# Performance work log

Measured on AMD Instinct MI355X. Metric: run time of the kernel, lower is better.

Reference implementation:

```python
import jax, jax.numpy as jnp
import numpy as np

B, S, D = 2, 2048, 2048
HQ, HK, HD = 16, 8, 128          # query heads, kv heads, head_dim
EPS = 1e-6
ROPE_THETA = 10000.0
SCALE = HD ** -0.5


def setup_inputs() -> dict:
    key = jax.random.key(0)
    ks = jax.random.split(key, 6)
    s = lambda fan_in: 1.0 / np.sqrt(fan_in)
    return {
        "hidden_states": jax.random.normal(ks[0], (B, S, D), jnp.float32),
        "positions": jnp.arange(S, dtype=jnp.int32),
        "Wq": jax.random.normal(ks[1], (D, HQ * HD), jnp.float32) * s(D),
        "Wk": jax.random.normal(ks[2], (D, HK * HD), jnp.float32) * s(D),
        "Wv": jax.random.normal(ks[3], (D, HK * HD), jnp.float32) * s(D),
        "Wo": jax.random.normal(ks[4], (HQ * HD, D), jnp.float32) * s(HQ * HD),
        "q_norm_w": jnp.ones((HD,), jnp.float32),
        "k_norm_w": jnp.ones((HD,), jnp.float32),
    }


def _rmsnorm(x, w):
    # RMSNorm over last (head_dim) axis, as in q_norm/k_norm
    var = jnp.mean(jnp.square(x), axis=-1, keepdims=True)
    return x * jax.lax.rsqrt(var + EPS) * w


def _rope(x, positions):
    # x: [B, S, H, HD]; rotate_half-style RoPE (Qwen3 convention)
    half = HD // 2
    inv_freq = 1.0 / (ROPE_THETA ** (jnp.arange(0, half, dtype=jnp.float32) / half))
    angles = positions.astype(jnp.float32)[:, None] * inv_freq[None, :]  # [S, half]
    cos = jnp.cos(angles)[None, :, None, :]  # [1, S, 1, half]
    sin = jnp.sin(angles)[None, :, None, :]
    x1, x2 = x[..., :half], x[..., half:]
    return jnp.concatenate([x1 * cos - x2 * sin, x2 * cos + x1 * sin], axis=-1)


def reference(hidden_states, positions, Wq, Wk, Wv, Wo, q_norm_w, k_norm_w):
    b, s, _ = hidden_states.shape
    q = (hidden_states @ Wq).reshape(b, s, HQ, HD)
    k = (hidden_states @ Wk).reshape(b, s, HK, HD)
    v = (hidden_states @ Wv).reshape(b, s, HK, HD)

    q = _rmsnorm(q, q_norm_w)
    k = _rmsnorm(k, k_norm_w)

    q = _rope(q, positions)
    k = _rope(k, positions)

    # GQA: repeat KV heads to match query heads
    groups = HQ // HK
    k = jnp.repeat(k, groups, axis=2)  # [B, S, HQ, HD]
    v = jnp.repeat(v, groups, axis=2)

    scores = jnp.einsum("bqhd,bkhd->bhqk", q, k) * SCALE  # [B, HQ, S, S]
    causal = jnp.tril(jnp.ones((s, s), dtype=bool))
    scores = jnp.where(causal[None, None], scores, jnp.float32(-jnp.inf))
    attn = jax.nn.softmax(scores, axis=-1)

    out = jnp.einsum("bhqk,bkhd->bqhd", attn, v).reshape(b, s, HQ * HD)
    return out @ Wo
```

## Files before the change

### kernel.cpp

```cpp
#include <hip/hip_runtime.h>
#include <cstdint>
#include <cstddef>

typedef _Float16 half8 __attribute__((ext_vector_type(8)));
typedef float f32x4 __attribute__((ext_vector_type(4)));

#define DI __device__ __forceinline__

DI void gld_lds16(void* sp, const void* gp) {
  __builtin_amdgcn_global_load_lds(
      (const __attribute__((address_space(1))) void*)gp,
      (__attribute__((address_space(3))) void*)sp, 16, 0, 0);
}

__global__ __launch_bounds__(256) void cvt_f32_f16(const float* __restrict__ in,
                                                   _Float16* __restrict__ outp, int n8) {
  const int i = blockIdx.x * 256 + threadIdx.x;
  if (i >= n8) return;
  const float4* p = (const float4*)in + (size_t)i * 2;
  const float4 a = p[0], b = p[1];
  half8 h;
  h[0] = (_Float16)a.x; h[1] = (_Float16)a.y; h[2] = (_Float16)a.z; h[3] = (_Float16)a.w;
  h[4] = (_Float16)b.x; h[5] = (_Float16)b.y; h[6] = (_Float16)b.z; h[7] = (_Float16)b.w;
  *(half8*)(outp + (size_t)i * 8) = h;
}

__global__ __launch_bounds__(256) void transpose_cvt(const float* __restrict__ in,
                                                     _Float16* __restrict__ outp,
                                                     int R, int C) {
  __shared__ float t[32][33];
  const int tx = threadIdx.x & 31, ty = threadIdx.x >> 5;
  const int ctiles = C >> 5;
  const int tc = blockIdx.x % ctiles, tr = blockIdx.x / ctiles;
  const int r0 = tr * 32, c0 = tc * 32;
#pragma unroll
  for (int i = 0; i < 4; i++)
    t[ty + 8 * i][tx] = in[(size_t)(r0 + ty + 8 * i) * C + c0 + tx];
  __syncthreads();
#pragma unroll
  for (int i = 0; i < 4; i++) {
    const int rr = ty + 8 * i;
    outp[(size_t)(c0 + rr) * R + r0 + tx] = (_Float16)t[tx][rr];
  }
}

__global__ __launch_bounds__(256) void gemm_bt(const _Float16* __restrict__ A,
                                               const _Float16* __restrict__ Bt,
                                               float* __restrict__ C,
                                               int M, int N, int K) {
  __shared__ _Float16 sA[2][128 * 32];
  __shared__ _Float16 sB[2][128 * 32];
  const int tid = threadIdx.x;
  const int w = tid >> 6, l = tid & 63, lo = l & 15, hi = l >> 4;
  const int bn0 = blockIdx.x * 128, bm0 = blockIdx.y * 128;
  const int wm = w >> 1, wn = w & 1;
  const int srow = l >> 2;
  const int scol = (l & 3) * 8;

  f32x4 acc[4][4];
#pragma unroll
  for (int mi = 0; mi < 4; mi++)
#pragma unroll
    for (int ni = 0; ni < 4; ni++)
#pragma unroll
      for (int r = 0; r < 4; r++) acc[mi][ni][r] = 0.0f;

  auto stage = [&](int bi, int kt) {
#pragma unroll
    for (int i = 0; i < 2; ++i) {
      const int j = 2 * w + i;
      gld_lds16(&sA[bi][j * 512],
                A + (size_t)(bm0 + j * 16 + srow) * K + (size_t)kt * 32 + scol);
      gld_lds16(&sB[bi][j * 512],
                Bt + (size_t)(bn0 + j * 16 + srow) * K + (size_t)kt * 32 + scol);
    }
  };

  stage(0, 0);
  __syncthreads();
  const int KT = K >> 5;
#pragma unroll 1
  for (int kt = 0; kt < KT; ++kt) {
    const int cur = kt & 1;
    if (kt + 1 < KT) stage(cur ^ 1, kt + 1);
    half8 a[4], b[4];
#pragma unroll
    for (int mi = 0; mi < 4; mi++)
      a[mi] = *(const half8*)&sA[cur][(wm * 64 + mi * 16 + lo) * 32 + hi * 8];
#pragma unroll
    for (int ni = 0; ni < 4; ni++)
      b[ni] = *(const half8*)&sB[cur][(wn * 64 + ni * 16 + lo) * 32 + hi * 8];
#pragma unroll
    for (int mi = 0; mi < 4; mi++)
#pragma unroll
      for (int ni = 0; ni < 4; ni++)
        acc[mi][ni] = __builtin_amdgcn_mfma_f32_16x16x32_f16(a[mi], b[ni], acc[mi][ni], 0, 0, 0);
    __syncthreads();
  }

#pragma unroll
  for (int mi = 0; mi < 4; mi++)
#pragma unroll
    for (int ni = 0; ni < 4; ni++)
#pragma unroll
      for (int r = 0; r < 4; r++)
        C[(size_t)(bm0 + wm * 64 + mi * 16 + hi * 4 + r) * N +
          (bn0 + wn * 64 + ni * 16 + lo)] = acc[mi][ni][r];
}

__global__ __launch_bounds__(256) void norm_rope(const float* __restrict__ QKV,
                                                 const int* __restrict__ pos,
                                                 const float* __restrict__ qw,
                                                 const float* __restrict__ kw,
                                                 _Float16* __restrict__ Qb,
                                                 _Float16* __restrict__ Kb) {
  const int w = threadIdx.x >> 6, l = threadIdx.x & 63;
  const int wv = blockIdx.x * 4 + w;
  const int t = wv / 24, hh = wv - t * 24;
  const int b = t >> 11, s = t & 2047;
  const bool isq = hh < 16;
  const int col = isq ? hh * 128 : 2048 + (hh - 16) * 128;
  const float* x = QKV + (size_t)t * 4096 + col;
  const float x1 = x[l], x2 = x[l + 64];
  float ss = x1 * x1 + x2 * x2;
  ss += __shfl_xor(ss, 32); ss += __shfl_xor(ss, 16); ss += __shfl_xor(ss, 8);
  ss += __shfl_xor(ss, 4);  ss += __shfl_xor(ss, 2);  ss += __shfl_xor(ss, 1);
  const float rn = rsqrtf(ss * 0.0078125f + 1e-6f);
  const float* wt = isq ? qw : kw;
  const float n1 = x1 * rn * wt[l], n2 = x2 * rn * wt[l + 64];
  const float ang = (float)pos[s] * exp2f((float)l * -0.2076205059304601f);
  float sa, ca;
  sincosf(ang, &sa, &ca);
  const float o1 = n1 * ca - n2 * sa;
  const float o2 = n2 * ca + n1 * sa;
  _Float16* dst = isq ? Qb + (((size_t)b * 16 + hh) * 2048 + s) * 128
                      : Kb + (((size_t)b * 8 + (hh - 16)) * 2048 + s) * 128;
  dst[l] = (_Float16)o1;
  dst[l + 64] = (_Float16)o2;
}

__global__ __launch_bounds__(256) void v_trans(const float* __restrict__ QKV,
                                               _Float16* __restrict__ Vt) {
  __shared__ float t[32][33];
  const int tx = threadIdx.x & 31, ty = threadIdx.x >> 5;
  const int dt = blockIdx.x & 3;
  const int st = (blockIdx.x >> 2) & 63;
  const int bh = blockIdx.x >> 8;
  const float* src = QKV + (size_t)((bh >> 3) * 2048 + st * 32) * 4096 +
                     3072 + (bh & 7) * 128 + dt * 32;
#pragma unroll
  for (int i = 0; i < 4; i++)
    t[ty + 8 * i][tx] = src[(size_t)(ty + 8 * i) * 4096 + tx];
  __syncthreads();
  _Float16* dst = Vt + ((size_t)bh * 128 + dt * 32) * 2048 + st * 32;
#pragma unroll
  for (int i = 0; i < 4; i++) {
    const int rr = ty + 8 * i;
    dst[(size_t)rr * 2048 + tx] = (_Float16)t[tx][rr];
  }
}

__global__ __launch_bounds__(256) void attn_fwd(const _Float16* __restrict__ Q,
                                                const _Float16* __restrict__ K,
                                                const _Float16* __restrict__ Vt,
                                                _Float16* __restrict__ AO) {
  __shared__ _Float16 sK[2][64 * 128];
  __shared__ _Float16 sV[2][128 * 64];
  __shared__ _Float16 P[4][16 * 80];
  const int tid = threadIdx.x, w = tid >> 6, l = tid & 63, lo = l & 15, hi = l >> 4;
  const int qt = 31 - (blockIdx.x >> 5);
  const int hq = blockIdx.x & 15;
  const int b = (blockIdx.x >> 4) & 1;
  const int hk = hq >> 1, q0 = qt * 64;
  const _Float16* Qh = Q + ((size_t)(b * 16 + hq) * 2048) * 128;
  const _Float16* Kh = K + ((size_t)(b * 8 + hk) * 2048) * 128;
  const _Float16* Vh = Vt + ((size_t)(b * 8 + hk) * 128) * 2048;
  const int qw0 = q0 + w * 16;

  auto stageK = [&](int bi, int kv0) {
#pragma unroll
    for (int i = 0; i < 4; ++i) {
      const int inst = w * 4 + i;
      const int r = inst * 4 + (l >> 4);
      const int cb = ((l & 15) * 16) ^ ((r & 7) << 4);
      gld_lds16(&sK[bi][inst * 512],
                (const char*)Kh + (size_t)(kv0 + r) * 256 + cb);
    }
  };
  auto stageV = [&](int bi, int kv0) {
#pragma unroll
    for (int i = 0; i < 4; ++i) {
      const int inst = w * 4 + i;
      const int r = inst * 8 + (l >> 3);
      const int cb = ((l & 7) * 16) ^ ((r & 7) << 4);
      gld_lds16(&sV[bi][inst * 512],
                (const char*)Vh + (size_t)r * 4096 + (size_t)kv0 * 2 + cb);
    }
  };

  half8 aq[4];
#pragma unroll
  for (int kc = 0; kc < 4; kc++)
    aq[kc] = *(const half8*)(Qh + (size_t)(qw0 + lo) * 128 + kc * 32 + hi * 8);

  f32x4 o[8];
#pragma unroll
  for (int dn = 0; dn < 8; dn++)
#pragma unroll
    for (int r = 0; r < 4; r++) o[dn][r] = 0.0f;
  float mrow[4], lrow[4];
#pragma unroll
  for (int r = 0; r < 4; r++) { mrow[r] = -1e30f; lrow[r] = 0.0f; }

  const int nt = qt + 1;
  stageK(0, 0);
  stageV(0, 0);
  __syncthreads();
#pragma unroll 1
  for (int kt = 0; kt < nt; ++kt) {
    const int kv0 = kt * 64;
    const int cur = kt & 1;
    if (kt + 1 < nt) {
      stageK(cur ^ 1, kv0 + 64);
      stageV(cur ^ 1, kv0 + 64);
    }
    const char* kb = (const char*)sK[cur];
    const char* vb = (const char*)sV[cur];
    f32x4 s[4];
#pragma unroll
    for (int ns = 0; ns < 4; ns++) {
#pragma unroll
      for (int r = 0; r < 4; r++) s[ns][r] = 0.0f;
      const int krow = ns * 16 + lo;
#pragma unroll
      for (int kc = 0; kc < 4; kc++) {
        half8 bk = *(const half8*)(kb + krow * 256 +
                                   ((kc * 64 + hi * 16) ^ ((krow & 7) << 4)));
        s[ns] = __builtin_amdgcn_mfma_f32_16x16x32_f16(aq[kc], bk, s[ns], 0, 0, 0);
      }
    }
    float tmax[4] = {-1e30f, -1e30f, -1e30f, -1e30f};
#pragma unroll
    for (int ns = 0; ns < 4; ns++) {
      const int kv = kv0 + ns * 16 + lo;
#pragma unroll
      for (int r = 0; r < 4; r++) {
        float v = s[ns][r] * 0.08838834764831845f;
        v = (kv <= qw0 + hi * 4 + r) ? v : -1e30f;
        s[ns][r] = v;
        tmax[r] = fmaxf(tmax[r], v);
      }
    }
#pragma unroll
    for (int r = 0; r < 4; r++) {
      tmax[r] = fmaxf(tmax[r], __shfl_xor(tmax[r], 1));
      tmax[r] = fmaxf(tmax[r], __shfl_xor(tmax[r], 2));
      tmax[r] = fmaxf(tmax[r], __shfl_xor(tmax[r], 4));
      tmax[r] = fmaxf(tmax[r], __shfl_xor(tmax[r], 8));
    }
    float corr[4], psum[4];
#pragma unroll
    for (int r = 0; r < 4; r++) {
      const float mn = fmaxf(mrow[r], tmax[r]);
      corr[r] = __expf(mrow[r] - mn);
      mrow[r] = mn;
      psum[r] = 0.0f;
    }
#pragma unroll
    for (int ns = 0; ns < 4; ns++)
#pragma unroll
      for (int r = 0; r < 4; r++) {
        const float p = __expf(s[ns][r] - mrow[r]);
        s[ns][r] = p;
        psum[r] += p;
      }
#pragma unroll
    for (int r = 0; r < 4; r++) {
      psum[r] += __shfl_xor(psum[r], 1);
      psum[r] += __shfl_xor(psum[r], 2);
      psum[r] += __shfl_xor(psum[r], 4);
      psum[r] += __shfl_xor(psum[r], 8);
      lrow[r] = lrow[r] * corr[r] + psum[r];
    }
#pragma unroll
    for (int dn = 0; dn < 8; dn++)
#pragma unroll
      for (int r = 0; r < 4; r++) o[dn][r] *= corr[r];
#pragma unroll
    for (int ns = 0; ns < 4; ns++)
#pragma unroll
      for (int r = 0; r < 4; r++)
        P[w][(hi * 4 + r) * 80 + ns * 16 + lo] = (_Float16)s[ns][r];
    asm volatile("s_waitcnt lgkmcnt(0)" ::: "memory");
    half8 ap0 = *(const half8*)&P[w][lo * 80 + hi * 8];
    half8 ap1 = *(const half8*)&P[w][lo * 80 + 32 + hi * 8];
#pragma unroll
    for (int dn = 0; dn < 8; dn++) {
      const int vrow = dn * 16 + lo;
      half8 bv0 = *(const half8*)(vb + vrow * 128 + ((hi * 16) ^ ((vrow & 7) << 4)));
      half8 bv1 = *(const half8*)(vb + vrow * 128 + ((64 + hi * 16) ^ ((vrow & 7) << 4)));
      o[dn] = __builtin_amdgcn_mfma_f32_16x16x32_f16(ap0, bv0, o[dn], 0, 0, 0);
      o[dn] = __builtin_amdgcn_mfma_f32_16x16x32_f16(ap1, bv1, o[dn], 0, 0, 0);
    }
    __syncthreads();
  }

  float inv[4];
#pragma unroll
  for (int r = 0; r < 4; r++) inv[r] = 1.0f / lrow[r];
  const size_t tok = (size_t)b * 2048 + qw0;
#pragma unroll
  for (int dn = 0; dn < 8; dn++)
#pragma unroll
    for (int r = 0; r < 4; r++)
      AO[(tok + hi * 4 + r) * 2048 + hq * 128 + dn * 16 + lo] = (_Float16)(o[dn][r] * inv[r]);
}

extern "C" void kernel_launch(void* const* d_in, const int* in_sizes, int n_in,
                              void* d_out, int out_size, void* d_ws, size_t ws_size,
                              hipStream_t stream) {
  (void)in_sizes; (void)n_in; (void)out_size; (void)ws_size;
  const float* hs  = (const float*)d_in[0];
  const int*   pos = (const int*)d_in[1];
  const float* Wq  = (const float*)d_in[2];
  const float* Wk  = (const float*)d_in[3];
  const float* Wv  = (const float*)d_in[4];
  const float* Wo  = (const float*)d_in[5];
  const float* qnw = (const float*)d_in[6];
  const float* knw = (const float*)d_in[7];
  float* out = (float*)d_out;

  char* ws = (char*)d_ws;
  size_t off = 0;
  auto take = [&](size_t bytes) -> void* {
    void* p = ws + off;
    off += (bytes + 255) & ~(size_t)255;
    return p;
  };
  _Float16* Xh    = (_Float16*)take((size_t)4096 * 2048 * 2);
  _Float16* Wqkvt = (_Float16*)take((size_t)4096 * 2048 * 2);
  _Float16* Wot   = (_Float16*)take((size_t)2048 * 2048 * 2);
  float*    QKV   = (float*)take((size_t)4096 * 4096 * 4);
  _Float16* Qb    = (_Float16*)take((size_t)2 * 16 * 2048 * 128 * 2);
  _Float16* Kb    = (_Float16*)take((size_t)2 * 8 * 2048 * 128 * 2);
  _Float16* Vt    = (_Float16*)take((size_t)2 * 8 * 128 * 2048 * 2);
  _Float16* AO    = (_Float16*)take((size_t)4096 * 2048 * 2);

  cvt_f32_f16<<<4096, 256, 0, stream>>>(hs, Xh, 1048576);
  transpose_cvt<<<64 * 64, 256, 0, stream>>>(Wq, Wqkvt, 2048, 2048);
  transpose_cvt<<<64 * 32, 256, 0, stream>>>(Wk, Wqkvt + (size_t)2048 * 2048, 2048, 1024);
  transpose_cvt<<<64 * 32, 256, 0, stream>>>(Wv, Wqkvt + (size_t)3072 * 2048, 2048, 1024);
  transpose_cvt<<<64 * 64, 256, 0, stream>>>(Wo, Wot, 2048, 2048);
  gemm_bt<<<dim3(32, 32), 256, 0, stream>>>(Xh, Wqkvt, QKV, 4096, 4096, 2048);
  norm_rope<<<24576, 256, 0, stream>>>(QKV, pos, qnw, knw, Qb, Kb);
  v_trans<<<4096, 256, 0, stream>>>(QKV, Vt);
  attn_fwd<<<1024, 256, 0, stream>>>(Qb, Kb, Vt, AO);
  gemm_bt<<<dim3(16, 32), 256, 0, stream>>>(AO, Wot, out, 4096, 2048, 2048);
}
```

Before: 285.0 us.

## Transpose score MFMA, fold softmax scale into Q, lazy rescale, remap GEMM tiles

The attention kernel now computes S^T so that each lane owns one query row. This removes the four-way per-row shuffle reductions and lets P be written to LDS as packed half4. The softmax scale and log2(e) are folded into Q in the norm/rope kernel so exp2f can be used directly. The causal mask is applied only on the diagonal tile, and the output rescale is skipped unless the running max grows by more than 8 (in log2 units), at some risk to fp16 range. The GEMM also remaps block IDs so that consecutive blocks are spread across XCDs.

```diff
diff --git a/kernel.cpp b/kernel.cpp
--- a/kernel.cpp
+++ b/kernel.cpp
@@ -3,6 +3,7 @@
 #include <cstddef>
 
 typedef _Float16 half8 __attribute__((ext_vector_type(8)));
+typedef _Float16 half4 __attribute__((ext_vector_type(4)));
 typedef float f32x4 __attribute__((ext_vector_type(4)));
 
 #define DI __device__ __forceinline__
@@ -52,7 +53,10 @@
   __shared__ _Float16 sB[2][128 * 32];
   const int tid = threadIdx.x;
   const int w = tid >> 6, l = tid & 63, lo = l & 15, hi = l >> 4;
-  const int bn0 = blockIdx.x * 128, bm0 = blockIdx.y * 128;
+  const int gx = gridDim.x, nwg = gx * gridDim.y;
+  int bid = blockIdx.y * gx + blockIdx.x;
+  bid = (bid & 7) * (nwg >> 3) + (bid >> 3);
+  const int bn0 = (bid % gx) * 128, bm0 = (bid / gx) * 128;
   const int wm = w >> 1, wn = w & 1;
   const int srow = l >> 2;
   const int scol = (l & 3) * 8;
@@ -131,8 +135,9 @@
   const float ang = (float)pos[s] * exp2f((float)l * -0.2076205059304601f);
   float sa, ca;
   sincosf(ang, &sa, &ca);
-  const float o1 = n1 * ca - n2 * sa;
-  const float o2 = n2 * ca + n1 * sa;
+  const float qs = isq ? 0.12751731f : 1.0f;
+  const float o1 = (n1 * ca - n2 * sa) * qs;
+  const float o2 = (n2 * ca + n1 * sa) * qs;
   _Float16* dst = isq ? Qb + (((size_t)b * 16 + hh) * 2048 + s) * 128
                       : Kb + (((size_t)b * 8 + (hh - 16)) * 2048 + s) * 128;
   dst[l] = (_Float16)o1;
@@ -208,9 +213,7 @@
   for (int dn = 0; dn < 8; dn++)
 #pragma unroll
     for (int r = 0; r < 4; r++) o[dn][r] = 0.0f;
-  float mrow[4], lrow[4];
-#pragma unroll
-  for (int r = 0; r < 4; r++) { mrow[r] = -1e30f; lrow[r] = 0.0f; }
+  float mrow = -1e30f, lrow = 0.0f;
 
   const int nt = qt + 1;
   stageK(0, 0);
@@ -236,61 +239,53 @@
       for (int kc = 0; kc < 4; kc++) {
         half8 bk = *(const half8*)(kb + krow * 256 +
                                    ((kc * 64 + hi * 16) ^ ((krow & 7) << 4)));
-        s[ns] = __builtin_amdgcn_mfma_f32_16x16x32_f16(aq[kc], bk, s[ns], 0, 0, 0);
+        s[ns] = __builtin_amdgcn_mfma_f32_16x16x32_f16(bk, aq[kc], s[ns], 0, 0, 0);
       }
     }
-    float tmax[4] = {-1e30f, -1e30f, -1e30f, -1e30f};
+    if (kt == nt - 1) {
+#pragma unroll
+      for (int ns = 0; ns < 4; ns++) {
+        const int kv = kv0 + ns * 16 + hi * 4;
+#pragma unroll
+        for (int r = 0; r < 4; r++)
+          if (kv + r > qw0 + lo) s[ns][r] = -1e30f;
+      }
+    }
+    float tmax = s[0][0];
+#pragma unroll
+    for (int ns = 0; ns < 4; ns++)
+#pragma unroll
+      for (int r = 0; r < 4; r++) tmax = fmaxf(tmax, s[ns][r]);
+    tmax = fmaxf(tmax, __shfl_xor(tmax, 16));
+    tmax = fmaxf(tmax, __shfl_xor(tmax, 32));
+    if (!__all(tmax <= mrow + 8.0f)) {
+      const float mn = fmaxf(mrow, tmax);
+      const float corr = exp2f(mrow - mn);
+      mrow = mn;
+      lrow *= corr;
+      float c4[4];
+#pragma unroll
+      for (int r = 0; r < 4; r++) c4[r] = __shfl(corr, hi * 4 + r, 16);
+#pragma unroll
+      for (int dn = 0; dn < 8; dn++)
+#pragma unroll
+        for (int r = 0; r < 4; r++) o[dn][r] *= c4[r];
+    }
+    float psum = 0.0f;
 #pragma unroll
     for (int ns = 0; ns < 4; ns++) {
-      const int kv = kv0 + ns * 16 + lo;
+      half4 pk;
 #pragma unroll
       for (int r = 0; r < 4; r++) {
-        float v = s[ns][r] * 0.08838834764831845f;
-        v = (kv <= qw0 + hi * 4 + r) ? v : -1e30f;
-        s[ns][r] = v;
-        tmax[r] = fmaxf(tmax[r], v);
+        const float p = exp2f(s[ns][r] - mrow);
+        psum += p;
+        pk[r] = (_Float16)p;
       }
-    }
-#pragma unroll
-    for (int r = 0; r < 4; r++) {
-      tmax[r] = fmaxf(tmax[r], __shfl_xor(tmax[r], 1));
-      tmax[r] = fmaxf(tmax[r], __shfl_xor(tmax[r], 2));
-      tmax[r] = fmaxf(tmax[r], __shfl_xor(tmax[r], 4));
-      tmax[r] = fmaxf(tmax[r], __shfl_xor(tmax[r], 8));
-    }
-    float corr[4], psum[4];
-#pragma unroll
-    for (int r = 0; r < 4; r++) {
-      const float mn = fmaxf(mrow[r], tmax[r]);
-      corr[r] = __expf(mrow[r] - mn);
-      mrow[r] = mn;
-      psum[r] = 0.0f;
-    }
-#pragma unroll
-    for (int ns = 0; ns < 4; ns++)
-#pragma unroll
-      for (int r = 0; r < 4; r++) {
-        const float p = __expf(s[ns][r] - mrow[r]);
-        s[ns][r] = p;
-        psum[r] += p;
-      }
-#pragma unroll
-    for (int r = 0; r < 4; r++) {
-      psum[r] += __shfl_xor(psum[r], 1);
-      psum[r] += __shfl_xor(psum[r], 2);
-      psum[r] += __shfl_xor(psum[r], 4);
-      psum[r] += __shfl_xor(psum[r], 8);
-      lrow[r] = lrow[r] * corr[r] + psum[r];
-    }
-#pragma unroll
-    for (int dn = 0; dn < 8; dn++)
-#pragma unroll
-      for (int r = 0; r < 4; r++) o[dn][r] *= corr[r];
-#pragma unroll
-    for (int ns = 0; ns < 4; ns++)
-#pragma unroll
-      for (int r = 0; r < 4; r++)
-        P[w][(hi * 4 + r) * 80 + ns * 16 + lo] = (_Float16)s[ns][r];
+      *(half4*)&P[w][lo * 80 + ns * 16 + hi * 4] = pk;
+    }
+    psum += __shfl_xor(psum, 16);
+    psum += __shfl_xor(psum, 32);
+    lrow += psum;
     asm volatile("s_waitcnt lgkmcnt(0)" ::: "memory");
     half8 ap0 = *(const half8*)&P[w][lo * 80 + hi * 8];
     half8 ap1 = *(const half8*)&P[w][lo * 80 + 32 + hi * 8];
@@ -305,15 +300,16 @@
     __syncthreads();
   }
 
-  float inv[4];
-#pragma unroll
-  for (int r = 0; r < 4; r++) inv[r] = 1.0f / lrow[r];
+  const float inv = 1.0f / lrow;
+  float i4[4];
+#pragma unroll
+  for (int r = 0; r < 4; r++) i4[r] = __shfl(inv, hi * 4 + r, 16);
   const size_t tok = (size_t)b * 2048 + qw0;
 #pragma unroll
   for (int dn = 0; dn < 8; dn++)
 #pragma unroll
     for (int r = 0; r < 4; r++)
-      AO[(tok + hi * 4 + r) * 2048 + hq * 128 + dn * 16 + lo] = (_Float16)(o[dn][r] * inv[r]);
+      AO[(tok + hi * 4 + r) * 2048 + hq * 128 + dn * 16 + lo] = (_Float16)(o[dn][r] * i4[r]);
 }
 
 extern "C" void kernel_launch(void* const* d_in, const int* in_sizes, int n_in,
```

Result: faster. 260.0 us (-8.8%).
